# Kernel optimization log

Measured on AMD Instinct MI355X. Metric: run time of the kernel, lower is better.

The kernel has to match this reference:

```python
import jax, jax.numpy as jnp
import numpy as np

B, N, DIN, DOUT, D, C = 64, 8192, 64, 64, 10, 4
NPC = N // C  # nodes per client


def setup_inputs() -> dict:
    key = jax.random.key(0)
    ks = jax.random.split(key, 6)
    x = jax.random.normal(ks[0], (B, N, DIN), dtype=jnp.float32)
    node_embeddings = jax.random.normal(ks[1], (N, D), dtype=jnp.float32)
    poly_coefficients = jax.random.normal(ks[2], (C, 1, 4), dtype=jnp.float32)  # unused in sprtrelu mode
    mask = jnp.ones((B, N, 1), dtype=jnp.float32)
    weights_pool = jax.random.normal(ks[3], (C, D, DIN, DOUT), dtype=jnp.float32)
    bias_pool = jax.random.normal(ks[4], (C, D, DOUT), dtype=jnp.float32)
    nodes_per = jnp.arange(N, dtype=jnp.int64 if jax.config.x64_enabled else jnp.int32).reshape(C, NPC)
    return {"x": x, "node_embeddings": node_embeddings, "poly_coefficients": poly_coefficients,
            "mask": mask, "weights_pool": weights_pool, "bias_pool": bias_pool, "nodes_per": nodes_per}


def reference(x, node_embeddings, poly_coefficients, mask, weights_pool, bias_pool, nodes_per):
    # active_mode='sprtrelu', inter_dropout=0.0 -> bernoulli mask is all ones,
    # so sum_EH is the sum of EH over ALL clients, identical for every client.
    c, n = nodes_per.shape
    b = x.shape[0]
    x = x * mask                                       # [B,N,Din]
    E = node_embeddings[nodes_per]                     # [C,n,D] client-wise gather
    xg = jnp.take(x, nodes_per.reshape(-1), axis=1).reshape(b, c, n, -1)  # [B,C,n,Din]
    tE = jax.nn.relu(E)                                # [C,n,D]
    # per-client EH_c = einsum('nd,bnc->bdc'); sum over clients (bernoulli all ones)
    sum_EH = jnp.einsum('cnd,bcni->bdi', tE, xg)       # [B,D,Din]
    # Z_c = H_c + transformed_E_c @ sum_EH
    Z = xg + jnp.einsum('cnd,bdi->bcni', tE, sum_EH)   # [B,C,n,Din]
    # dynamic per-node weights/bias from embeddings
    W = jnp.einsum('cnd,cdio->cnio', E, weights_pool)  # [C,n,Din,Dout]
    bb = jnp.einsum('cnd,cdo->cno', E, bias_pool)      # [C,n,Dout]
    out = jnp.einsum('bcni,cnio->bcno', Z, W) + bb     # [B,C,n,Dout]
    return out.reshape(b, c * n, -1)                   # concat over clients along node dim
```

## Files before the change

kernel.cpp:

```cpp
#include <hip/hip_runtime.h>
#include <hip/hip_bf16.h>


#define BB 64
#define NN 8192
#define DI 64
#define DO 64
#define DD 10
#define CC 4
#define NPC 2048

typedef __bf16 bf16;
typedef __bf16 bf16x8 __attribute__((ext_vector_type(8)));
typedef float f32x4 __attribute__((ext_vector_type(4)));

__global__ __launch_bounds__(256) void k_sumEH(
    const float* __restrict__ x, const float* __restrict__ emb,
    const float* __restrict__ mask, const int* __restrict__ np,
    float* __restrict__ sEH) {
  const int b = blockIdx.x >> 4;
  const int chunk = blockIdx.x & 15;
  const int lane = threadIdx.x & 63;
  const int w = threadIdx.x >> 6;

  float acc[DD];
#pragma unroll
  for (int d = 0; d < DD; ++d) acc[d] = 0.f;

  const float* xb = x + (size_t)b * NN * DI;
  const float* mb = mask + (size_t)b * NN;

  for (int nn = 0; nn < 128; ++nn) {
    const int pos = chunk * 512 + nn * 4 + w;
    const int node = np[pos];
    const float m = mb[node];
    const float xv = xb[(size_t)node * DI + lane] * m;
    const float2* e2 = (const float2*)(emb + (size_t)node * DD);
    float2 e0 = e2[0], e1 = e2[1], e4 = e2[2], e6 = e2[3], e8 = e2[4];
    acc[0] = fmaf(fmaxf(e0.x, 0.f), xv, acc[0]);
    acc[1] = fmaf(fmaxf(e0.y, 0.f), xv, acc[1]);
    acc[2] = fmaf(fmaxf(e1.x, 0.f), xv, acc[2]);
    acc[3] = fmaf(fmaxf(e1.y, 0.f), xv, acc[3]);
    acc[4] = fmaf(fmaxf(e4.x, 0.f), xv, acc[4]);
    acc[5] = fmaf(fmaxf(e4.y, 0.f), xv, acc[5]);
    acc[6] = fmaf(fmaxf(e6.x, 0.f), xv, acc[6]);
    acc[7] = fmaf(fmaxf(e6.y, 0.f), xv, acc[7]);
    acc[8] = fmaf(fmaxf(e8.x, 0.f), xv, acc[8]);
    acc[9] = fmaf(fmaxf(e8.y, 0.f), xv, acc[9]);
  }

  __shared__ float red[4][DD][64];
#pragma unroll
  for (int d = 0; d < DD; ++d) red[w][d][lane] = acc[d];
  __syncthreads();

  for (int t = threadIdx.x; t < DD * 64; t += 256) {
    const int d = t >> 6, i = t & 63;
    const float s = red[0][d][i] + red[1][d][i] + red[2][d][i] + red[3][d][i];
    atomicAdd(sEH + ((size_t)b * DD + d) * 64 + i, s);
  }
}

__global__ __launch_bounds__(256) void k_main(
    const float* __restrict__ x, const float* __restrict__ emb,
    const float* __restrict__ mask, const float* __restrict__ wp,
    const float* __restrict__ bp, const int* __restrict__ np,
    const float* __restrict__ sEH, float* __restrict__ out) {
  __shared__ float E_l[4][DD];
  __shared__ float tE_l[4][DD];
  __shared__ float bb_l[4][64];
  __shared__ float mask_l[64][4];
  __shared__ __align__(16) bf16 Wt[4][64][72];
  __shared__ __align__(16) bf16 Zl[16][4][72];

  const int tid = threadIdx.x;
  const int lane = tid & 63;
  const int w = tid >> 6;
  const int p0 = blockIdx.x * 4;
  const int c = p0 >> 11;

  int node[4];
#pragma unroll
  for (int g = 0; g < 4; ++g) node[g] = np[p0 + g];

  if (tid < 40) {
    const int g = tid / 10, d = tid % 10;
    const float e = emb[(size_t)node[g] * DD + d];
    E_l[g][d] = e;
    tE_l[g][d] = fmaxf(e, 0.f);
  }
  {
    const int b = tid >> 2, g = tid & 3;
    mask_l[b][g] = mask[(size_t)b * NN + node[g]];
  }
  __syncthreads();

  {
    float acc = 0.f;
#pragma unroll
    for (int d = 0; d < DD; ++d)
      acc = fmaf(E_l[w][d], bp[((size_t)(c * DD + d)) * DO + lane], acc);
    bb_l[w][lane] = acc;
  }

  {
    float accW0[16], accW1[16], accW2[16], accW3[16];
#pragma unroll
    for (int p = 0; p < 16; ++p) { accW0[p] = 0.f; accW1[p] = 0.f; accW2[p] = 0.f; accW3[p] = 0.f; }
#pragma unroll
    for (int d = 0; d < DD; ++d) {
      const float e0 = E_l[0][d], e1 = E_l[1][d], e2 = E_l[2][d], e3 = E_l[3][d];
      const float* wrow = wp + ((size_t)(c * DD + d) * DI + w * 16) * DO + lane;
#pragma unroll
      for (int p = 0; p < 16; ++p) {
        const float v = wrow[(size_t)p * DO];
        accW0[p] = fmaf(e0, v, accW0[p]);
        accW1[p] = fmaf(e1, v, accW1[p]);
        accW2[p] = fmaf(e2, v, accW2[p]);
        accW3[p] = fmaf(e3, v, accW3[p]);
      }
    }
    float* accs[4] = {accW0, accW1, accW2, accW3};
#pragma unroll
    for (int g = 0; g < 4; ++g) {
      bf16x8 v0, v1;
#pragma unroll
      for (int p = 0; p < 8; ++p) { v0[p] = (bf16)accs[g][p]; v1[p] = (bf16)accs[g][p + 8]; }
      *(bf16x8*)&Wt[g][lane][w * 16] = v0;
      *(bf16x8*)&Wt[g][lane][w * 16 + 8] = v1;
    }
  }

  float tEr[4][DD];
#pragma unroll
  for (int g = 0; g < 4; ++g)
#pragma unroll
    for (int d = 0; d < DD; ++d) tEr[g][d] = tE_l[g][d];
  __syncthreads();

  for (int chunk = 0; chunk < 4; ++chunk) {
#pragma unroll
    for (int bb4 = 0; bb4 < 4; ++bb4) {
      const int b_loc = w * 4 + bb4;
      const int b = chunk * 16 + b_loc;
      float z0 = x[((size_t)b * NN + node[0]) * DI + lane] * mask_l[b][0];
      float z1 = x[((size_t)b * NN + node[1]) * DI + lane] * mask_l[b][1];
      float z2 = x[((size_t)b * NN + node[2]) * DI + lane] * mask_l[b][2];
      float z3 = x[((size_t)b * NN + node[3]) * DI + lane] * mask_l[b][3];
      const float* sb = sEH + (size_t)b * DD * 64 + lane;
#pragma unroll
      for (int d = 0; d < DD; ++d) {
        const float s = sb[(size_t)d * 64];
        z0 = fmaf(tEr[0][d], s, z0);
        z1 = fmaf(tEr[1][d], s, z1);
        z2 = fmaf(tEr[2][d], s, z2);
        z3 = fmaf(tEr[3][d], s, z3);
      }
      Zl[b_loc][0][lane] = (bf16)z0;
      Zl[b_loc][1][lane] = (bf16)z1;
      Zl[b_loc][2][lane] = (bf16)z2;
      Zl[b_loc][3][lane] = (bf16)z3;
    }
    __syncthreads();

    {
      const int g = w;
      const int q = lane >> 4, r16 = lane & 15;
      f32x4 acc[4];
#pragma unroll
      for (int nt = 0; nt < 4; ++nt) {
        const float bv = bb_l[g][nt * 16 + r16];
        acc[nt][0] = bv; acc[nt][1] = bv; acc[nt][2] = bv; acc[nt][3] = bv;
      }
#pragma unroll
      for (int kt = 0; kt < 2; ++kt) {
        const int k0 = kt * 32 + q * 8;
        const bf16x8 a = *(const bf16x8*)&Zl[r16][g][k0];
#pragma unroll
        for (int nt = 0; nt < 4; ++nt) {
          const bf16x8 bf = *(const bf16x8*)&Wt[g][nt * 16 + r16][k0];
          acc[nt] = __builtin_amdgcn_mfma_f32_16x16x32_bf16(a, bf, acc[nt], 0, 0, 0);
        }
      }
      const size_t pg = (size_t)(p0 + g);
#pragma unroll
      for (int nt = 0; nt < 4; ++nt) {
#pragma unroll
        for (int r = 0; r < 4; ++r) {
          const int bg = chunk * 16 + q * 4 + r;
          out[((size_t)bg * NN + pg) * DO + nt * 16 + r16] = acc[nt][r];
        }
      }
    }
    __syncthreads();
  }
}

extern "C" void kernel_launch(void* const* d_in, const int* in_sizes, int n_in,
                              void* d_out, int out_size, void* d_ws, size_t ws_size,
                              hipStream_t stream) {
  const float* x    = (const float*)d_in[0];
  const float* emb  = (const float*)d_in[1];
  const float* mask = (const float*)d_in[3];
  const float* wp   = (const float*)d_in[4];
  const float* bp   = (const float*)d_in[5];
  const int*   np   = (const int*)d_in[6];
  float* out = (float*)d_out;
  float* sEH = (float*)d_ws;

  hipMemsetAsync(sEH, 0, (size_t)BB * DD * 64 * sizeof(float), stream);
  k_sumEH<<<dim3(BB * 16), dim3(256), 0, stream>>>(x, emb, mask, np, sEH);
  k_main<<<dim3(NN / 4), dim3(256), 0, stream>>>(x, emb, mask, wp, bp, np, sEH, out);
}
```

Measured before the change: 368.1 us.

## Vectorize x loads with float4 and stage embeddings in LDS for sumEH

k_sumEH now preloads node indices, masks and masked relu embeddings into shared memory. Each lane then reads float4 slices of x, with four nodes handled per wave instead of one, and the partial sums are reduced with cross-lane shuffles. In k_main the Z construction uses float4 loads of x and sEH, with each lane covering a node/column-quad pair. The per-thread tEr register copy is dropped, and the LDS padding for Wt/Zl changes from 72 to 80. The aim is fewer, wider global loads and lower register pressure, at the cost of extra LDS traffic and reductions.

After: 437.6 us. +18.9%, slower.

```diff
diff --git a/kernel.cpp b/kernel.cpp
--- a/kernel.cpp
+++ b/kernel.cpp
@@ -12,52 +12,79 @@
 
 typedef __bf16 bf16;
 typedef __bf16 bf16x8 __attribute__((ext_vector_type(8)));
+typedef __bf16 bf16x4 __attribute__((ext_vector_type(4)));
 typedef float f32x4 __attribute__((ext_vector_type(4)));
 
 __global__ __launch_bounds__(256) void k_sumEH(
     const float* __restrict__ x, const float* __restrict__ emb,
     const float* __restrict__ mask, const int* __restrict__ np,
     float* __restrict__ sEH) {
+  __shared__ int np_l[512];
+  __shared__ float mask_l[512];
+  __shared__ float tEm[512][DD];
+  __shared__ __align__(16) float red[4][DD][64];
+
   const int b = blockIdx.x >> 4;
   const int chunk = blockIdx.x & 15;
-  const int lane = threadIdx.x & 63;
-  const int w = threadIdx.x >> 6;
-
-  float acc[DD];
-#pragma unroll
-  for (int d = 0; d < DD; ++d) acc[d] = 0.f;
-
-  const float* xb = x + (size_t)b * NN * DI;
-  const float* mb = mask + (size_t)b * NN;
-
-  for (int nn = 0; nn < 128; ++nn) {
-    const int pos = chunk * 512 + nn * 4 + w;
-    const int node = np[pos];
-    const float m = mb[node];
-    const float xv = xb[(size_t)node * DI + lane] * m;
-    const float2* e2 = (const float2*)(emb + (size_t)node * DD);
-    float2 e0 = e2[0], e1 = e2[1], e4 = e2[2], e6 = e2[3], e8 = e2[4];
-    acc[0] = fmaf(fmaxf(e0.x, 0.f), xv, acc[0]);
-    acc[1] = fmaf(fmaxf(e0.y, 0.f), xv, acc[1]);
-    acc[2] = fmaf(fmaxf(e1.x, 0.f), xv, acc[2]);
-    acc[3] = fmaf(fmaxf(e1.y, 0.f), xv, acc[3]);
-    acc[4] = fmaf(fmaxf(e4.x, 0.f), xv, acc[4]);
-    acc[5] = fmaf(fmaxf(e4.y, 0.f), xv, acc[5]);
-    acc[6] = fmaf(fmaxf(e6.x, 0.f), xv, acc[6]);
-    acc[7] = fmaf(fmaxf(e6.y, 0.f), xv, acc[7]);
-    acc[8] = fmaf(fmaxf(e8.x, 0.f), xv, acc[8]);
-    acc[9] = fmaf(fmaxf(e8.y, 0.f), xv, acc[9]);
-  }
-
-  __shared__ float red[4][DD][64];
-#pragma unroll
-  for (int d = 0; d < DD; ++d) red[w][d][lane] = acc[d];
-  __syncthreads();
-
-  for (int t = threadIdx.x; t < DD * 64; t += 256) {
-    const int d = t >> 6, i = t & 63;
-    const float s = red[0][d][i] + red[1][d][i] + red[2][d][i] + red[3][d][i];
-    atomicAdd(sEH + ((size_t)b * DD + d) * 64 + i, s);
+  const int tid = threadIdx.x;
+  const int lane = tid & 63;
+  const int w = tid >> 6;
+
+  for (int s = tid; s < 512; s += 256) {
+    const int node = np[chunk * 512 + s];
+    np_l[s] = node;
+    mask_l[s] = mask[(size_t)b * NN + node];
+  }
+  __syncthreads();
+  for (int s = tid; s < 2560; s += 256) {
+    const int nl = s / 5, pr = s % 5;
+    const float2 e = *(const float2*)(emb + (size_t)np_l[nl] * DD + pr * 2);
+    const float m = mask_l[nl];
+    tEm[nl][pr * 2] = fmaxf(e.x, 0.f) * m;
+    tEm[nl][pr * 2 + 1] = fmaxf(e.y, 0.f) * m;
+  }
+  __syncthreads();
+
+  const int qq = lane >> 4, r16 = lane & 15;
+  const f32x4* x4 = (const f32x4*)(x + (size_t)b * NN * DI);
+  f32x4 acc[DD];
+#pragma unroll
+  for (int d = 0; d < DD; ++d) acc[d] = (f32x4)0.f;
+
+  const int wbase = w * 128;
+#pragma unroll 4
+  for (int g = 0; g < 32; ++g) {
+    const int nl = wbase + g * 4 + qq;
+    const int node = np_l[nl];
+    const f32x4 xv = x4[(size_t)node * 16 + r16];
+#pragma unroll
+    for (int d = 0; d < DD; ++d) {
+      acc[d] += xv * tEm[nl][d];
+    }
+  }
+
+#pragma unroll
+  for (int d = 0; d < DD; ++d) {
+    f32x4 a = acc[d];
+#pragma unroll
+    for (int j = 0; j < 4; ++j) {
+      float v = a[j];
+      v += __shfl_xor(v, 16);
+      v += __shfl_xor(v, 32);
+      a[j] = v;
+    }
+    acc[d] = a;
+  }
+  if (qq == 0) {
+#pragma unroll
+    for (int d = 0; d < DD; ++d) *(f32x4*)&red[w][d][r16 * 4] = acc[d];
+  }
+  __syncthreads();
+
+  for (int s = tid; s < DD * 64; s += 256) {
+    const int d = s >> 6, i = s & 63;
+    const float v = red[0][d][i] + red[1][d][i] + red[2][d][i] + red[3][d][i];
+    atomicAdd(sEH + ((size_t)b * DD + d) * 64 + i, v);
   }
 }
 
@@ -70,8 +97,9 @@
   __shared__ float tE_l[4][DD];
   __shared__ float bb_l[4][64];
   __shared__ float mask_l[64][4];
-  __shared__ __align__(16) bf16 Wt[4][64][72];
-  __shared__ __align__(16) bf16 Zl[16][4][72];
+  __shared__ int node_l[4];
+  __shared__ __align__(16) bf16 Wt[4][64][80];
+  __shared__ __align__(16) bf16 Zl[16][4][80];
 
   const int tid = threadIdx.x;
   const int lane = tid & 63;
@@ -79,19 +107,16 @@
   const int p0 = blockIdx.x * 4;
   const int c = p0 >> 11;
 
-  int node[4];
-#pragma unroll
-  for (int g = 0; g < 4; ++g) node[g] = np[p0 + g];
-
+  if (tid < 4) node_l[tid] = np[p0 + tid];
   if (tid < 40) {
     const int g = tid / 10, d = tid % 10;
-    const float e = emb[(size_t)node[g] * DD + d];
+    const float e = emb[(size_t)np[p0 + g] * DD + d];
     E_l[g][d] = e;
     tE_l[g][d] = fmaxf(e, 0.f);
   }
   {
-    const int b = tid >> 2, g = tid & 3;
-    mask_l[b][g] = mask[(size_t)b * NN + node[g]];
+    const int bq = tid >> 2, g = tid & 3;
+    mask_l[bq][g] = mask[(size_t)bq * NN + np[p0 + g]];
   }
   __syncthreads();
 
@@ -104,62 +129,46 @@
   }
 
   {
-    float accW0[16], accW1[16], accW2[16], accW3[16];
-#pragma unroll
-    for (int p = 0; p < 16; ++p) { accW0[p] = 0.f; accW1[p] = 0.f; accW2[p] = 0.f; accW3[p] = 0.f; }
+    f32x4 accW[16];
+#pragma unroll
+    for (int p = 0; p < 16; ++p) accW[p] = (f32x4)0.f;
 #pragma unroll
     for (int d = 0; d < DD; ++d) {
-      const float e0 = E_l[0][d], e1 = E_l[1][d], e2 = E_l[2][d], e3 = E_l[3][d];
+      f32x4 ev;
+      ev[0] = E_l[0][d]; ev[1] = E_l[1][d]; ev[2] = E_l[2][d]; ev[3] = E_l[3][d];
       const float* wrow = wp + ((size_t)(c * DD + d) * DI + w * 16) * DO + lane;
 #pragma unroll
-      for (int p = 0; p < 16; ++p) {
-        const float v = wrow[(size_t)p * DO];
-        accW0[p] = fmaf(e0, v, accW0[p]);
-        accW1[p] = fmaf(e1, v, accW1[p]);
-        accW2[p] = fmaf(e2, v, accW2[p]);
-        accW3[p] = fmaf(e3, v, accW3[p]);
-      }
-    }
-    float* accs[4] = {accW0, accW1, accW2, accW3};
+      for (int p = 0; p < 16; ++p) accW[p] += ev * wrow[(size_t)p * DO];
+    }
 #pragma unroll
     for (int g = 0; g < 4; ++g) {
       bf16x8 v0, v1;
 #pragma unroll
-      for (int p = 0; p < 8; ++p) { v0[p] = (bf16)accs[g][p]; v1[p] = (bf16)accs[g][p + 8]; }
+      for (int p = 0; p < 8; ++p) { v0[p] = (bf16)accW[p][g]; v1[p] = (bf16)accW[p + 8][g]; }
       *(bf16x8*)&Wt[g][lane][w * 16] = v0;
       *(bf16x8*)&Wt[g][lane][w * 16 + 8] = v1;
     }
   }
 
-  float tEr[4][DD];
-#pragma unroll
-  for (int g = 0; g < 4; ++g)
-#pragma unroll
-    for (int d = 0; d < DD; ++d) tEr[g][d] = tE_l[g][d];
-  __syncthreads();
+  const int gq = lane >> 4, i4 = lane & 15;
+  const f32x4* x4 = (const f32x4*)x;
+  const f32x4* s4 = (const f32x4*)sEH;
 
   for (int chunk = 0; chunk < 4; ++chunk) {
 #pragma unroll
     for (int bb4 = 0; bb4 < 4; ++bb4) {
       const int b_loc = w * 4 + bb4;
       const int b = chunk * 16 + b_loc;
-      float z0 = x[((size_t)b * NN + node[0]) * DI + lane] * mask_l[b][0];
-      float z1 = x[((size_t)b * NN + node[1]) * DI + lane] * mask_l[b][1];
-      float z2 = x[((size_t)b * NN + node[2]) * DI + lane] * mask_l[b][2];
-      float z3 = x[((size_t)b * NN + node[3]) * DI + lane] * mask_l[b][3];
-      const float* sb = sEH + (size_t)b * DD * 64 + lane;
-#pragma unroll
-      for (int d = 0; d < DD; ++d) {
-        const float s = sb[(size_t)d * 64];
-        z0 = fmaf(tEr[0][d], s, z0);
-        z1 = fmaf(tEr[1][d], s, z1);
-        z2 = fmaf(tEr[2][d], s, z2);
-        z3 = fmaf(tEr[3][d], s, z3);
-      }
-      Zl[b_loc][0][lane] = (bf16)z0;
-      Zl[b_loc][1][lane] = (bf16)z1;
-      Zl[b_loc][2][lane] = (bf16)z2;
-      Zl[b_loc][3][lane] = (bf16)z3;
+      const int nd = node_l[gq];
+      f32x4 z = x4[((size_t)b * NN + nd) * 16 + i4];
+      z *= mask_l[b][gq];
+      const f32x4* sb = s4 + (size_t)b * DD * 16 + i4;
+#pragma unroll
+      for (int d = 0; d < DD; ++d) z += sb[d * 16] * tE_l[gq][d];
+      bf16x4 zb;
+#pragma unroll
+      for (int j = 0; j < 4; ++j) zb[j] = (bf16)z[j];
+      *(bf16x4*)&Zl[b_loc][gq][i4 * 4] = zb;
     }
     __syncthreads();
 
@@ -178,8 +187,8 @@
         const bf16x8 a = *(const bf16x8*)&Zl[r16][g][k0];
 #pragma unroll
         for (int nt = 0; nt < 4; ++nt) {
-          const bf16x8 bf = *(const bf16x8*)&Wt[g][nt * 16 + r16][k0];
-          acc[nt] = __builtin_amdgcn_mfma_f32_16x16x32_bf16(a, bf, acc[nt], 0, 0, 0);
+          const bf16x8 bfr = *(const bf16x8*)&Wt[g][nt * 16 + r16][k0];
+          acc[nt] = __builtin_amdgcn_mfma_f32_16x16x32_bf16(a, bfr, acc[nt], 0, 0, 0);
         }
       }
       const size_t pg = (size_t)(p0 + g);
```
